# Kernel optimization log

Measured on AMD Instinct MI355X. Metric: run time of the kernel, lower is better.

## Reference

```python
import jax, jax.numpy as jnp
import numpy as np

SEM_ENC_DIM = 1024
SENT_HIDDEN_DIM = 1024
ATT_DIM = 512

def setup_inputs() -> dict:
    key = jax.random.key(0)
    ks = jax.random.split(key, 8)
    B, L = 64, 2048
    s = lambda d: 1.0 / np.sqrt(d)
    return {
        "sem_enc_output": jax.random.normal(ks[0], (B, L, SEM_ENC_DIM), dtype=jnp.float32),
        "dec_hidden_state": jax.random.normal(ks[1], (B, SENT_HIDDEN_DIM), dtype=jnp.float32),
        "W_enc": jax.random.uniform(ks[2], (SEM_ENC_DIM, ATT_DIM), jnp.float32, -s(SEM_ENC_DIM), s(SEM_ENC_DIM)),
        "b_enc": jax.random.uniform(ks[3], (ATT_DIM,), jnp.float32, -s(SEM_ENC_DIM), s(SEM_ENC_DIM)),
        "W_dec": jax.random.uniform(ks[4], (SENT_HIDDEN_DIM, ATT_DIM), jnp.float32, -s(SENT_HIDDEN_DIM), s(SENT_HIDDEN_DIM)),
        "b_dec": jax.random.uniform(ks[5], (ATT_DIM,), jnp.float32, -s(SENT_HIDDEN_DIM), s(SENT_HIDDEN_DIM)),
        "W_full": jax.random.uniform(ks[6], (ATT_DIM, 1), jnp.float32, -s(ATT_DIM), s(ATT_DIM)),
        "b_full": jax.random.uniform(ks[7], (1,), jnp.float32, -s(ATT_DIM), s(ATT_DIM)),
    }

def reference(sem_enc_output, dec_hidden_state, W_enc, b_enc, W_dec, b_dec, W_full, b_full):
    # enc projection: [B, L, att_dim]
    enc_proj = jnp.einsum('ble,ea->bla', sem_enc_output, W_enc) + b_enc
    # dec projection: [B, att_dim]
    dec_proj = dec_hidden_state @ W_dec + b_dec
    # broadcast add + tanh: [B, L, att_dim]
    joined = jnp.tanh(enc_proj + dec_proj[:, None, :])
    # scoring: [B, L]
    scores = (jnp.einsum('bla,a->bl', joined, W_full[:, 0]) + b_full[0])
    att_scores = jax.nn.softmax(scores, axis=1)
    # weighted sum over L of the PROJECTED encoder output (matches torch code)
    att_output = jnp.einsum('bl,bla->ba', att_scores, enc_proj)
    return (att_output, att_scores)
```

## Files before the change

kernel.cpp:

```cpp
#include <hip/hip_runtime.h>
#include <hip/hip_bf16.h>
#include <cstdint>
#include <cstddef>

#define BB   64
#define LL   2048
#define ED   1024
#define AD   512
#define BM   64
#define BK   32
#define NCH  (LL / BM)
#define KST  (ED / BK)

typedef short  short8  __attribute__((ext_vector_type(8)));
typedef float  f32x4   __attribute__((ext_vector_type(4)));

__device__ __forceinline__ unsigned short f2bf(float x) {
  unsigned u = __float_as_uint(x);
  u += 0x7FFFu + ((u >> 16) & 1u);
  return (unsigned short)(u >> 16);
}

#define GLOAD_LDS16(gp, lp)                                                        \
  __builtin_amdgcn_global_load_lds(                                                \
      (const __attribute__((address_space(1))) unsigned int*)(gp),                 \
      (__attribute__((address_space(3))) unsigned int*)(lp), 16, 0, 0)

__global__ __launch_bounds__(512) void prep_kernel(
    const float* __restrict__ W_enc, const float* __restrict__ dec,
    const float* __restrict__ W_dec, const float* __restrict__ b_dec,
    unsigned short* __restrict__ Wb, float* __restrict__ dp) {
  const int blk = blockIdx.x, t = threadIdx.x;
  if (blk < BB) {
    const float* drow = dec + blk * ED;
    float a0 = 0.f, a1 = 0.f, a2 = 0.f, a3 = 0.f;
    for (int k = 0; k < ED; k += 4) {
      a0 = fmaf(drow[k],     W_dec[(k)     * AD + t], a0);
      a1 = fmaf(drow[k + 1], W_dec[(k + 1) * AD + t], a1);
      a2 = fmaf(drow[k + 2], W_dec[(k + 2) * AD + t], a2);
      a3 = fmaf(drow[k + 3], W_dec[(k + 3) * AD + t], a3);
    }
    dp[blk * AD + t] = (a0 + a1) + (a2 + a3) + b_dec[t];
  } else {
    const int base = (blk - BB) * 4096;
#pragma unroll
    for (int ii = 0; ii < 8; ii++) {
      const int o    = base + ii * 512 + t;
      const int ks   = o >> 14;
      const int cblk = (o >> 9) & 31;
      const int kg   = (o >> 7) & 3;
      const int r    = (o >> 3) & 15;
      const int j    = o & 7;
      const int k    = ks * 32 + kg * 8 + j;
      const int c    = cblk * 16 + r;
      Wb[o] = f2bf(W_enc[k * AD + c]);
    }
  }
}

__global__ __launch_bounds__(256, 2) void fused_kernel(
    const float* __restrict__ sem, const unsigned short* __restrict__ Wb,
    const float* __restrict__ dp, const float* __restrict__ b_enc,
    const float* __restrict__ Wf,
    float* __restrict__ raw_scores,
    float* __restrict__ ws_ms, float* __restrict__ ws_o) {

  __shared__ unsigned short Alds[2][2048];
  __shared__ unsigned short Blds[2][16384];

  const int t    = threadIdx.x;
  const int lane = t & 63;
  const int wn   = t >> 6;
  const int b    = blockIdx.y;
  const int chunk= blockIdx.x;
  const int l0   = chunk * BM;

  const int srow = t >> 2;
  const int skg  = t & 3;
  const float* aptr = sem + ((size_t)(b * LL + l0 + srow)) * ED + skg * 8;
  const unsigned short* bsrc = Wb + t * 8;
  const int awr = (srow >> 4) * 512 + skg * 128 + (srow & 15) * 8;

  const int arow = lane & 15;
  const int akg  = lane >> 4;
  const int afr  = lane * 8;
  const int bfr  = wn * 8 * 512 + lane * 8;

  f32x4 acc[4][8];
#pragma unroll
  for (int i = 0; i < 4; i++)
#pragma unroll
    for (int j = 0; j < 8; j++) acc[i][j] = (f32x4)0.f;

#pragma unroll
  for (int i = 0; i < 8; i++)
    GLOAD_LDS16(bsrc + i * 2048, &Blds[0][i * 2048 + t * 8]);
  f32x4 pA0 = *(const f32x4*)(aptr);
  f32x4 pA1 = *(const f32x4*)(aptr + 4);
  f32x4 qA0 = *(const f32x4*)(aptr + BK);
  f32x4 qA1 = *(const f32x4*)(aptr + BK + 4);
  {
    short8 aw;
    aw[0]=(short)f2bf(pA0[0]); aw[1]=(short)f2bf(pA0[1]); aw[2]=(short)f2bf(pA0[2]); aw[3]=(short)f2bf(pA0[3]);
    aw[4]=(short)f2bf(pA1[0]); aw[5]=(short)f2bf(pA1[1]); aw[6]=(short)f2bf(pA1[2]); aw[7]=(short)f2bf(pA1[3]);
    *(short8*)&Alds[0][awr] = aw;
  }
  asm volatile("s_waitcnt vmcnt(2) lgkmcnt(0)" ::: "memory");
  __builtin_amdgcn_sched_barrier(0);
  __builtin_amdgcn_s_barrier();

#define ITER(ks, CA0, CA1, LA0, LA1)                                              \
  {                                                                               \
    const int cb = (ks) & 1, nb = ((ks) + 1) & 1;                                 \
    if ((ks) + 1 < KST) {                      \
      const unsigned short* bs = bsrc + ((ks) + 1) * 16384;                       \
      _Pragma("unroll")                                                           \
      for (int i = 0; i < 8; i++)                                                 \
        GLOAD_LDS16(bs + i * 2048, &Blds[nb][i * 2048 + t * 8]);                  \
    }                                                                             \
    __builtin_amdgcn_sched_barrier(0);  \
    if ((ks) + 1 < KST) {                                                         \
      short8 aw;                                                                  \
      aw[0]=(short)f2bf(CA0[0]); aw[1]=(short)f2bf(CA0[1]);                       \
      aw[2]=(short)f2bf(CA0[2]); aw[3]=(short)f2bf(CA0[3]);                       \
      aw[4]=(short)f2bf(CA1[0]); aw[5]=(short)f2bf(CA1[1]);                       \
      aw[6]=(short)f2bf(CA1[2]); aw[7]=(short)f2bf(CA1[3]);                       \
      *(short8*)&Alds[nb][awr] = aw;                                              \
    }                                                                             \
    if ((ks) + 2 < KST) {                                                         \
      const float* ap = aptr + ((ks) + 2) * BK;                                   \
      LA0 = *(const f32x4*)(ap);                                                  \
      LA1 = *(const f32x4*)(ap + 4);                                              \
    }                                                                             \
    short8 av[4], bv[8];                                                          \
    _Pragma("unroll")                                                             \
    for (int mf = 0; mf < 4; mf++)                                                \
      av[mf] = *(const short8*)&Alds[cb][afr + mf * 512];                         \
    _Pragma("unroll")                                                             \
    for (int nf = 0; nf < 8; nf++)                                                \
      bv[nf] = *(const short8*)&Blds[cb][bfr + nf * 512];                         \
    __builtin_amdgcn_s_setprio(1);                                                \
    _Pragma("unroll")                                                             \
    for (int mf = 0; mf < 4; mf++)                                                \
      _Pragma("unroll")                                                           \
      for (int nf = 0; nf < 8; nf++)                                              \
        acc[mf][nf] = __builtin_amdgcn_mfma_f32_16x16x32_bf16(av[mf], bv[nf], acc[mf][nf], 0, 0, 0); \
    __builtin_amdgcn_s_setprio(0);                                                \
    if ((ks) + 2 < KST) {                 \
      asm volatile("s_waitcnt vmcnt(2) lgkmcnt(0)" ::: "memory");                 \
    } else {                                                                      \
      asm volatile("s_waitcnt vmcnt(0) lgkmcnt(0)" ::: "memory");                 \
    }                                                                             \
    __builtin_amdgcn_sched_barrier(0);                                            \
    __builtin_amdgcn_s_barrier();                                                 \
  }

  for (int kk = 0; kk < KST; kk += 2) {
    ITER(kk,     qA0, qA1, pA0, pA1);
    ITER(kk + 1, pA0, pA1, qA0, qA1);
  }
#undef ITER

  float* eb = (float*)&Blds[0][0];
  float (*sc_part)[4] = (float (*)[4])eb;
  float* weight       = eb + 256;
  float* scores_lds   = eb + 320;

  float dpv[8], wfv[8], bev[8];
#pragma unroll
  for (int nf = 0; nf < 8; nf++) {
    const int c = wn * 128 + nf * 16 + arow;
    dpv[nf] = dp[b * AD + c];
    wfv[nf] = Wf[c];
    bev[nf] = b_enc[c];
  }
#pragma unroll
  for (int mf = 0; mf < 4; mf++) {
#pragma unroll
    for (int r = 0; r < 4; r++) {
      float p = 0.f;
#pragma unroll
      for (int nf = 0; nf < 8; nf++) {
        float e = acc[mf][nf][r] + bev[nf];
        acc[mf][nf][r] = e;
        float x = e + dpv[nf];
        float ex = __expf(2.f * x);
        float th = 1.f - 2.f / (ex + 1.f);
        p = fmaf(th, wfv[nf], p);
      }
      p += __shfl_xor(p, 1); p += __shfl_xor(p, 2);
      p += __shfl_xor(p, 4); p += __shfl_xor(p, 8);
      if (arow == 0) sc_part[mf * 16 + akg * 4 + r][wn] = p;
    }
  }
  __syncthreads();

  if (t < BM) {
    float s = sc_part[t][0] + sc_part[t][1] + sc_part[t][2] + sc_part[t][3];
    raw_scores[(size_t)b * LL + l0 + t] = s;
    float m = s;
#pragma unroll
    for (int off = 1; off < 64; off <<= 1) m = fmaxf(m, __shfl_xor(m, off));
    float w = __expf(s - m);
    weight[t] = w;
    float ss = w;
#pragma unroll
    for (int off = 1; off < 64; off <<= 1) ss += __shfl_xor(ss, off);
    if (t == 0) {
      ws_ms[(b * NCH + chunk) * 2]     = m;
      ws_ms[(b * NCH + chunk) * 2 + 1] = ss;
    }
  }
  __syncthreads();

  float wv[4][4];
#pragma unroll
  for (int mf = 0; mf < 4; mf++)
#pragma unroll
    for (int r = 0; r < 4; r++) wv[mf][r] = weight[mf * 16 + akg * 4 + r];
#pragma unroll
  for (int nf = 0; nf < 8; nf++) {
    float cp = 0.f;
#pragma unroll
    for (int mf = 0; mf < 4; mf++)
#pragma unroll
      for (int r = 0; r < 4; r++) cp = fmaf(wv[mf][r], acc[mf][nf][r], cp);
    cp += __shfl_xor(cp, 16);
    cp += __shfl_xor(cp, 32);
    if (lane < 16)
      ws_o[((size_t)b * NCH + chunk) * AD + wn * 128 + nf * 16 + lane] = cp;
  }
}

__global__ __launch_bounds__(256) void finalize_kernel(
    const float* __restrict__ ws_ms, const float* __restrict__ ws_o,
    float* __restrict__ out0, float* __restrict__ outS) {
  const int b = blockIdx.x, t = threadIdx.x;
  float ms[NCH], ss[NCH];
  float M = -1e30f;
#pragma unroll
  for (int i = 0; i < NCH; i++) {
    ms[i] = ws_ms[(b * NCH + i) * 2];
    ss[i] = ws_ms[(b * NCH + i) * 2 + 1];
    M = fmaxf(M, ms[i]);
  }
  float S = 0.f, w[NCH];
#pragma unroll
  for (int i = 0; i < NCH; i++) { w[i] = __expf(ms[i] - M); S = fmaf(ss[i], w[i], S); }
  const float invS = 1.f / S;
  for (int c = t; c < AD; c += 256) {
    float a = 0.f;
#pragma unroll
    for (int i = 0; i < NCH; i++) a = fmaf(ws_o[((size_t)b * NCH + i) * AD + c], w[i], a);
    out0[b * AD + c] = a * invS;
  }
  for (int l = t; l < LL; l += 256) {
    float r = outS[(size_t)b * LL + l];
    outS[(size_t)b * LL + l] = __expf(r - M) * invS;
  }
}

extern "C" void kernel_launch(void* const* d_in, const int* in_sizes, int n_in,
                              void* d_out, int out_size, void* d_ws, size_t ws_size,
                              hipStream_t stream) {
  const float* sem    = (const float*)d_in[0];
  const float* dec    = (const float*)d_in[1];
  const float* W_enc  = (const float*)d_in[2];
  const float* b_enc  = (const float*)d_in[3];
  const float* W_dec  = (const float*)d_in[4];
  const float* b_dec  = (const float*)d_in[5];
  const float* W_full = (const float*)d_in[6];

  float* out0 = (float*)d_out;
  float* outS = out0 + BB * AD;

  char* ws = (char*)d_ws;
  unsigned short* Wb = (unsigned short*)ws;
  float* dpw   = (float*)(ws + (1 << 20));
  float* ws_ms = (float*)(ws + (1 << 20) + (128 << 10));
  float* ws_o  = (float*)(ws + (1 << 20) + (144 << 10));

  prep_kernel<<<BB + 128, 512, 0, stream>>>(W_enc, dec, W_dec, b_dec, Wb, dpw);
  dim3 g1(NCH, BB);
  fused_kernel<<<g1, 256, 0, stream>>>(sem, Wb, dpw, b_enc, W_full, outS, ws_ms, ws_o);
  finalize_kernel<<<BB, 256, 0, stream>>>(ws_ms, ws_o, out0, outS);
}
```

Measured before the change: 283.6 us.

## Use 8 waves per block with narrower per-wave N tiles and packed bf16 conversion

Result: no change. 278.9 us (-1.6%).

```diff
diff --git a/kernel.cpp b/kernel.cpp
--- a/kernel.cpp
+++ b/kernel.cpp
@@ -8,10 +8,10 @@
 #define ED   1024
 #define AD   512
 #define BM   64
-#define BK   32
 #define NCH  (LL / BM)
-#define KST  (ED / BK)
-
+#define KST  32
+
+typedef short  short4v __attribute__((ext_vector_type(4)));
 typedef short  short8  __attribute__((ext_vector_type(8)));
 typedef float  f32x4   __attribute__((ext_vector_type(4)));
 
@@ -19,6 +19,13 @@
   unsigned u = __float_as_uint(x);
   u += 0x7FFFu + ((u >> 16) & 1u);
   return (unsigned short)(u >> 16);
+}
+
+__device__ __forceinline__ short4v cvt4(f32x4 v) {
+  union { short4v s; unsigned u[2]; } r;
+  asm("v_cvt_pk_bf16_f32 %0, %1, %2" : "=v"(r.u[0]) : "v"(v[0]), "v"(v[1]));
+  asm("v_cvt_pk_bf16_f32 %0, %1, %2" : "=v"(r.u[1]) : "v"(v[2]), "v"(v[3]));
+  return r.s;
 }
 
 #define GLOAD_LDS16(gp, lp)                                                        \
@@ -58,15 +65,15 @@
   }
 }
 
-__global__ __launch_bounds__(256, 2) void fused_kernel(
+__global__ __launch_bounds__(512, 4) void fused_kernel(
     const float* __restrict__ sem, const unsigned short* __restrict__ Wb,
     const float* __restrict__ dp, const float* __restrict__ b_enc,
     const float* __restrict__ Wf,
     float* __restrict__ raw_scores,
     float* __restrict__ ws_ms, float* __restrict__ ws_o) {
 
-  __shared__ unsigned short Alds[2][2048];
-  __shared__ unsigned short Blds[2][16384];
+  __shared__ unsigned short Ab[2][2048];
+  __shared__ unsigned short Bb[2][16384];
 
   const int t    = threadIdx.x;
   const int lane = t & 63;
@@ -75,101 +82,85 @@
   const int chunk= blockIdx.x;
   const int l0   = chunk * BM;
 
-  const int srow = t >> 2;
-  const int skg  = t & 3;
-  const float* aptr = sem + ((size_t)(b * LL + l0 + srow)) * ED + skg * 8;
+  const int srow = t >> 3;
+  const int skg  = t & 7;
+  const float* aptr = sem + ((size_t)(b * LL + l0 + srow)) * ED + skg * 4;
+  const int awr = (srow >> 4) * 512 + (skg >> 1) * 128 + (srow & 15) * 8 + (skg & 1) * 4;
+
   const unsigned short* bsrc = Wb + t * 8;
-  const int awr = (srow >> 4) * 512 + skg * 128 + (srow & 15) * 8;
 
   const int arow = lane & 15;
   const int akg  = lane >> 4;
   const int afr  = lane * 8;
-  const int bfr  = wn * 8 * 512 + lane * 8;
-
-  f32x4 acc[4][8];
+  const int bfr  = wn * 2048 + lane * 8;
+
+  f32x4 acc[4][4];
 #pragma unroll
   for (int i = 0; i < 4; i++)
 #pragma unroll
-    for (int j = 0; j < 8; j++) acc[i][j] = (f32x4)0.f;
-
-#pragma unroll
-  for (int i = 0; i < 8; i++)
-    GLOAD_LDS16(bsrc + i * 2048, &Blds[0][i * 2048 + t * 8]);
-  f32x4 pA0 = *(const f32x4*)(aptr);
-  f32x4 pA1 = *(const f32x4*)(aptr + 4);
-  f32x4 qA0 = *(const f32x4*)(aptr + BK);
-  f32x4 qA1 = *(const f32x4*)(aptr + BK + 4);
-  {
-    short8 aw;
-    aw[0]=(short)f2bf(pA0[0]); aw[1]=(short)f2bf(pA0[1]); aw[2]=(short)f2bf(pA0[2]); aw[3]=(short)f2bf(pA0[3]);
-    aw[4]=(short)f2bf(pA1[0]); aw[5]=(short)f2bf(pA1[1]); aw[6]=(short)f2bf(pA1[2]); aw[7]=(short)f2bf(pA1[3]);
-    *(short8*)&Alds[0][awr] = aw;
-  }
-  asm volatile("s_waitcnt vmcnt(2) lgkmcnt(0)" ::: "memory");
+    for (int j = 0; j < 4; j++) acc[i][j] = (f32x4)0.f;
+
+#pragma unroll
+  for (int i = 0; i < 4; i++)
+    GLOAD_LDS16(bsrc + i * 4096, &Bb[0][i * 4096 + t * 8]);
+  f32x4 pA = *(const f32x4*)(aptr);
+  f32x4 qA = *(const f32x4*)(aptr + 32);
+  *(short4v*)&Ab[0][awr] = cvt4(pA);
+  asm volatile("s_waitcnt vmcnt(1) lgkmcnt(0)" ::: "memory");
   __builtin_amdgcn_sched_barrier(0);
   __builtin_amdgcn_s_barrier();
 
-#define ITER(ks, CA0, CA1, LA0, LA1)                                              \
-  {                                                                               \
-    const int cb = (ks) & 1, nb = ((ks) + 1) & 1;                                 \
-    if ((ks) + 1 < KST) {                      \
-      const unsigned short* bs = bsrc + ((ks) + 1) * 16384;                       \
-      _Pragma("unroll")                                                           \
-      for (int i = 0; i < 8; i++)                                                 \
-        GLOAD_LDS16(bs + i * 2048, &Blds[nb][i * 2048 + t * 8]);                  \
-    }                                                                             \
-    __builtin_amdgcn_sched_barrier(0);  \
-    if ((ks) + 1 < KST) {                                                         \
-      short8 aw;                                                                  \
-      aw[0]=(short)f2bf(CA0[0]); aw[1]=(short)f2bf(CA0[1]);                       \
-      aw[2]=(short)f2bf(CA0[2]); aw[3]=(short)f2bf(CA0[3]);                       \
-      aw[4]=(short)f2bf(CA1[0]); aw[5]=(short)f2bf(CA1[1]);                       \
-      aw[6]=(short)f2bf(CA1[2]); aw[7]=(short)f2bf(CA1[3]);                       \
-      *(short8*)&Alds[nb][awr] = aw;                                              \
-    }                                                                             \
-    if ((ks) + 2 < KST) {                                                         \
-      const float* ap = aptr + ((ks) + 2) * BK;                                   \
-      LA0 = *(const f32x4*)(ap);                                                  \
-      LA1 = *(const f32x4*)(ap + 4);                                              \
-    }                                                                             \
-    short8 av[4], bv[8];                                                          \
-    _Pragma("unroll")                                                             \
-    for (int mf = 0; mf < 4; mf++)                                                \
-      av[mf] = *(const short8*)&Alds[cb][afr + mf * 512];                         \
-    _Pragma("unroll")                                                             \
-    for (int nf = 0; nf < 8; nf++)                                                \
-      bv[nf] = *(const short8*)&Blds[cb][bfr + nf * 512];                         \
-    __builtin_amdgcn_s_setprio(1);                                                \
-    _Pragma("unroll")                                                             \
-    for (int mf = 0; mf < 4; mf++)                                                \
-      _Pragma("unroll")                                                           \
-      for (int nf = 0; nf < 8; nf++)                                              \
+#define ITER(ks, CA, LA)                                                           \
+  {                                                                                \
+    const int cb = (ks) & 1, nb = ((ks) + 1) & 1;                                  \
+    if ((ks) + 1 < KST) {                                                          \
+      const unsigned short* bs = bsrc + ((ks) + 1) * 16384;                        \
+      _Pragma("unroll")                                                            \
+      for (int i = 0; i < 4; i++)                                                  \
+        GLOAD_LDS16(bs + i * 4096, &Bb[nb][i * 4096 + t * 8]);                     \
+    }                                                                              \
+    __builtin_amdgcn_sched_barrier(0);          \
+    if ((ks) + 1 < KST)                                                            \
+      *(short4v*)&Ab[nb][awr] = cvt4(CA);          \
+    if ((ks) + 2 < KST)                                                            \
+      LA = *(const f32x4*)(aptr + ((ks) + 2) * 32);                                \
+    short8 av[4], bv[4];                                                           \
+    _Pragma("unroll")                                                              \
+    for (int mf = 0; mf < 4; mf++)                                                 \
+      av[mf] = *(const short8*)&Ab[cb][afr + mf * 512];                            \
+    _Pragma("unroll")                                                              \
+    for (int nf = 0; nf < 4; nf++)                                                 \
+      bv[nf] = *(const short8*)&Bb[cb][bfr + nf * 512];                            \
+    __builtin_amdgcn_s_setprio(1);                                                 \
+    _Pragma("unroll")                                                              \
+    for (int mf = 0; mf < 4; mf++)                                                 \
+      _Pragma("unroll")                                                            \
+      for (int nf = 0; nf < 4; nf++)                                               \
         acc[mf][nf] = __builtin_amdgcn_mfma_f32_16x16x32_bf16(av[mf], bv[nf], acc[mf][nf], 0, 0, 0); \
-    __builtin_amdgcn_s_setprio(0);                                                \
-    if ((ks) + 2 < KST) {                 \
-      asm volatile("s_waitcnt vmcnt(2) lgkmcnt(0)" ::: "memory");                 \
-    } else {                                                                      \
-      asm volatile("s_waitcnt vmcnt(0) lgkmcnt(0)" ::: "memory");                 \
-    }                                                                             \
-    __builtin_amdgcn_sched_barrier(0);                                            \
-    __builtin_amdgcn_s_barrier();                                                 \
+    __builtin_amdgcn_s_setprio(0);                                                 \
+    if ((ks) + 2 < KST) {                                                          \
+      asm volatile("s_waitcnt vmcnt(1) lgkmcnt(0)" ::: "memory");                  \
+    } else {                                                                       \
+      asm volatile("s_waitcnt vmcnt(0) lgkmcnt(0)" ::: "memory");                  \
+    }                                                                              \
+    __builtin_amdgcn_sched_barrier(0);                                             \
+    __builtin_amdgcn_s_barrier();                                                  \
   }
 
   for (int kk = 0; kk < KST; kk += 2) {
-    ITER(kk,     qA0, qA1, pA0, pA1);
-    ITER(kk + 1, pA0, pA1, qA0, qA1);
+    ITER(kk,     qA, pA);
+    ITER(kk + 1, pA, qA);
   }
 #undef ITER
 
-  float* eb = (float*)&Blds[0][0];
-  float (*sc_part)[4] = (float (*)[4])eb;
-  float* weight       = eb + 256;
-  float* scores_lds   = eb + 320;
-
-  float dpv[8], wfv[8], bev[8];
-#pragma unroll
-  for (int nf = 0; nf < 8; nf++) {
-    const int c = wn * 128 + nf * 16 + arow;
+  float* eb = (float*)&Bb[0][0];
+  float (*sc_part)[8] = (float (*)[8])eb;
+  float* weight       = eb + 512;
+
+  float dpv[4], wfv[4], bev[4];
+#pragma unroll
+  for (int nf = 0; nf < 4; nf++) {
+    const int c = wn * 64 + nf * 16 + arow;
     dpv[nf] = dp[b * AD + c];
     wfv[nf] = Wf[c];
     bev[nf] = b_enc[c];
@@ -180,7 +171,7 @@
     for (int r = 0; r < 4; r++) {
       float p = 0.f;
 #pragma unroll
-      for (int nf = 0; nf < 8; nf++) {
+      for (int nf = 0; nf < 4; nf++) {
         float e = acc[mf][nf][r] + bev[nf];
         acc[mf][nf][r] = e;
         float x = e + dpv[nf];
@@ -196,7 +187,8 @@
   __syncthreads();
 
   if (t < BM) {
-    float s = sc_part[t][0] + sc_part[t][1] + sc_part[t][2] + sc_part[t][3];
+    float s = sc_part[t][0] + sc_part[t][1] + sc_part[t][2] + sc_part[t][3]
+            + sc_part[t][4] + sc_part[t][5] + sc_part[t][6] + sc_part[t][7];
     raw_scores[(size_t)b * LL + l0 + t] = s;
     float m = s;
 #pragma unroll
@@ -219,7 +211,7 @@
 #pragma unroll
     for (int r = 0; r < 4; r++) wv[mf][r] = weight[mf * 16 + akg * 4 + r];
 #pragma unroll
-  for (int nf = 0; nf < 8; nf++) {
+  for (int nf = 0; nf < 4; nf++) {
     float cp = 0.f;
 #pragma unroll
     for (int mf = 0; mf < 4; mf++)
@@ -228,7 +220,7 @@
     cp += __shfl_xor(cp, 16);
     cp += __shfl_xor(cp, 32);
     if (lane < 16)
-      ws_o[((size_t)b * NCH + chunk) * AD + wn * 128 + nf * 16 + lane] = cp;
+      ws_o[((size_t)b * NCH + chunk) * AD + wn * 64 + nf * 16 + lane] = cp;
   }
 }
 
@@ -282,6 +274,6 @@
 
   prep_kernel<<<BB + 128, 512, 0, stream>>>(W_enc, dec, W_dec, b_dec, Wb, dpw);
   dim3 g1(NCH, BB);
-  fused_kernel<<<g1, 256, 0, stream>>>(sem, Wb, dpw, b_enc, W_full, outS, ws_ms, ws_o);
+  fused_kernel<<<g1, 512, 0, stream>>>(sem, Wb, dpw, b_enc, W_full, outS, ws_ms, ws_o);
   finalize_kernel<<<BB, 256, 0, stream>>>(ws_ms, ws_o, out0, outS);
 }
```
